# Kernel optimization log

Hardware: AMD Instinct MI355X
Metric: run time of the kernel (lower is better)

## Reference

```python
import jax, jax.numpy as jnp
import numpy as np

NUM_HEADS = 8
ATTENTION_SPAN = 128
LOOKAHEAD = True
NEG_INF = -1e9  # tf.keras Softmax mask adder


def setup_inputs() -> dict:
    key = jax.random.key(0)
    k1, k2, k3 = jax.random.split(key, 3)
    B, S, D = 4, 2048, 512
    x = jax.random.normal(k1, (B, S, D), dtype=jnp.float32)
    w_qkv = jax.random.normal(k2, (D, 3 * D), dtype=jnp.float32) * (D ** -0.5)
    w_proj = jax.random.normal(k3, (D, D), dtype=jnp.float32) * (D ** -0.5)
    return {"x": x, "w_qkv": w_qkv, "w_proj": w_proj}


def _band_mask(S: int) -> jnp.ndarray:
    idx = jnp.arange(S)
    m = jnp.abs(idx[None, :] - idx[:, None]) <= ATTENTION_SPAN
    if not LOOKAHEAD:
        m = m & (idx[None, :] <= idx[:, None])
    return m  # [S, S] bool


def reference(x, w_qkv, w_proj):
    B, S, D = x.shape
    H = NUM_HEADS
    hd = D // H
    scale = D ** -0.5  # NOTE: source scales by full dim, not head_dim

    qkv = x @ w_qkv                                   # [B,S,3D]
    qkv = qkv.reshape(B, S, H, 3 * hd).transpose(0, 2, 1, 3)  # [B,H,S,3hd]
    q, k, v = jnp.split(qkv, 3, axis=-1)              # each [B,H,S,hd]

    scores = jnp.einsum('bhqd,bhkd->bhqk', q, k) * scale  # [B,H,S,S]
    mask = _band_mask(S)[None, None, :, :]
    scores = scores + (1.0 - mask.astype(scores.dtype)) * NEG_INF
    attn = jax.nn.softmax(scores, axis=-1)

    out = jnp.einsum('bhqk,bhkd->bhqd', attn, v)      # [B,H,S,hd]
    out = out.transpose(0, 2, 1, 3).reshape(B, S, D)
    return out @ w_proj
```

## Files before the change

### kernel.cpp

```cpp
#include <hip/hip_runtime.h>

typedef unsigned short u16;
typedef unsigned long long u64;
typedef __attribute__((ext_vector_type(8))) short s16x8;
typedef __attribute__((ext_vector_type(4))) float f32x4;

#define MFMA16(a, b, c) __builtin_amdgcn_mfma_f32_16x16x32_bf16((a), (b), (c), 0, 0, 0)

__device__ __forceinline__ u16 f2bf(float f) {
  unsigned u = __float_as_uint(f);
  u += 0x7fffu + ((u >> 16) & 1u);
  return (u16)(u >> 16);
}

__device__ __forceinline__ void gld_lds16(const void* g, void* l) {
  __builtin_amdgcn_global_load_lds(
      (const __attribute__((address_space(1))) void*)g,
      (__attribute__((address_space(3))) void*)l, 16, 0, 0);
}

__global__ __launch_bounds__(256) void prep(const float* __restrict__ X,
                                            const float* __restrict__ Wqkv,
                                            const float* __restrict__ Wproj,
                                            u16* __restrict__ Xb,
                                            u16* __restrict__ wqT,
                                            u16* __restrict__ wpT) {
  const int bid = blockIdx.x;
  if (bid < 2048) {
    size_t idx = (size_t)bid * 256 + threadIdx.x;
    const float4 f0 = *(const float4*)(X + idx * 8);
    const float4 f1 = *(const float4*)(X + idx * 8 + 4);
    float fs[8] = {f0.x, f0.y, f0.z, f0.w, f1.x, f1.y, f1.z, f1.w};
    s16x8 hv;
#pragma unroll
    for (int j = 0; j < 8; ++j) hv[j] = (short)f2bf(fs[j]);
    *(s16x8*)(Xb + idx * 8) = hv;
  } else if (bid < 2432) {
    int idx = (bid - 2048) * 256 + threadIdx.x;
    int n = idx % 1536;
    int kc = idx / 1536;
    int t = n >> 9, ct = n & 511, h = ct >> 6, d = ct & 63;
    int src_c = h * 192 + t * 64 + d;
    s16x8 hv;
#pragma unroll
    for (int i = 0; i < 8; ++i) hv[i] = (short)f2bf(Wqkv[(size_t)(kc * 8 + i) * 1536 + src_c]);
    *(s16x8*)(wqT + (size_t)n * 512 + (size_t)kc * 8) = hv;
  } else {
    int idx = (bid - 2432) * 256 + threadIdx.x;
    int n = idx % 512;
    int kc = idx / 512;
    s16x8 hv;
#pragma unroll
    for (int i = 0; i < 8; ++i) hv[i] = (short)f2bf(Wproj[(size_t)(kc * 8 + i) * 512 + n]);
    *(s16x8*)(wpT + (size_t)n * 512 + (size_t)kc * 8) = hv;
  }
}

template <int EPI, int NCOL>
__global__ __launch_bounds__(256, 2) void gemm_bf16(
    const u16* __restrict__ A, const u16* __restrict__ B,
    float* __restrict__ OUT,
    u16* __restrict__ qo, u16* __restrict__ ko, u16* __restrict__ vto) {
  __shared__ u16 LDS[32768];
  u16* SA = LDS;
  u16* SB = LDS + 16384;
  const int tid = threadIdx.x;
  const int w = tid >> 6, lane = tid & 63;
  const int l15 = lane & 15, l4 = lane >> 4;
  const int bid0 = blockIdx.x;
  const int work = (bid0 & 7) * (8 * NCOL) + (bid0 >> 3);
  const int bx = work / NCOL;
  const int by = work % NCOL;
  const int row0 = bx * 128;
  const int col0 = by * 128;
  const int wr = w >> 1, wc = w & 1;

  const int lrow = lane >> 3, lslot = lane & 7;
  const int srcoff = lrow * 1024 + ((lslot ^ lrow) << 4);
  const char* pA = (const char*)A + (size_t)(row0 + w * 32) * 1024 + srcoff;
  const char* pB = (const char*)B + (size_t)(col0 + w * 32) * 1024 + srcoff;
  u16* sAw = SA + (w * 32) * 64;
  u16* sBw = SB + (w * 32) * 64;

#define STAGE(t_, b_)                                               \
  do {                                                              \
    const int kbb = (t_)*128;                                       \
    _Pragma("unroll")                                               \
    for (int j = 0; j < 4; ++j) {                                   \
      gld_lds16(pA + j * 8192 + kbb, sAw + (b_)*8192 + j * 512);    \
      gld_lds16(pB + j * 8192 + kbb, sBw + (b_)*8192 + j * 512);    \
    }                                                               \
  } while (0)

  const f32x4 fz = {0.f, 0.f, 0.f, 0.f};
  f32x4 acc[4][4];
  for (int a = 0; a < 4; ++a)
    for (int b = 0; b < 4; ++b) acc[a][b] = fz;

  STAGE(0, 0);
  asm volatile("s_waitcnt vmcnt(0)" ::: "memory");
  __builtin_amdgcn_sched_barrier(0);
  __builtin_amdgcn_s_barrier();

  for (int t = 0; t < 8; ++t) {
    const int cur = t & 1;
    if (t + 1 < 8) STAGE(t + 1, cur ^ 1);
#pragma unroll
    for (int ks = 0; ks < 2; ++ks) {
      s16x8 af[4], bf[4];
#pragma unroll
      for (int mi = 0; mi < 4; ++mi) {
        const int r = wr * 64 + mi * 16 + l15;
        const int sl = (ks * 4 + l4) ^ (r & 7);
        af[mi] = *(const s16x8*)&SA[cur * 8192 + r * 64 + sl * 8];
      }
#pragma unroll
      for (int nj = 0; nj < 4; ++nj) {
        const int r = wc * 64 + nj * 16 + l15;
        const int sl = (ks * 4 + l4) ^ (r & 7);
        bf[nj] = *(const s16x8*)&SB[cur * 8192 + r * 64 + sl * 8];
      }
      __builtin_amdgcn_s_setprio(1);
#pragma unroll
      for (int nj = 0; nj < 4; ++nj)
#pragma unroll
        for (int mi = 0; mi < 4; ++mi) acc[mi][nj] = MFMA16(af[mi], bf[nj], acc[mi][nj]);
      __builtin_amdgcn_s_setprio(0);
    }
    if (t < 7) {
      asm volatile("s_waitcnt vmcnt(0)" ::: "memory");
      __builtin_amdgcn_sched_barrier(0);
      __builtin_amdgcn_s_barrier();
    }
  }
#undef STAGE

  if (EPI == 0) {
#pragma unroll
    for (int mi = 0; mi < 4; ++mi)
#pragma unroll
      for (int nj = 0; nj < 4; ++nj)
#pragma unroll
        for (int rg = 0; rg < 4; ++rg) {
          int r_g = row0 + wr * 64 + mi * 16 + l4 * 4 + rg;
          int c_g = col0 + wc * 64 + nj * 16 + l15;
          OUT[(size_t)r_g * 512 + c_g] = acc[mi][nj][rg];
        }
    return;
  }

  const int b = row0 >> 11, srow = row0 & 2047;
  if (by < 8) {
    const int isq = (by < 4);
    const float QS = 0.06375874f;
    u16* dst = isq ? qo : ko;
#pragma unroll
    for (int mi = 0; mi < 4; ++mi)
#pragma unroll
      for (int nj = 0; nj < 4; ++nj)
#pragma unroll
        for (int rg = 0; rg < 4; ++rg) {
          float v = acc[mi][nj][rg];
          if (isq) v *= QS;
          int s = srow + wr * 64 + mi * 16 + l4 * 4 + rg;
          int ct = ((by & 3) * 128 + wc * 64 + nj * 16 + l15);
          int h = ct >> 6, d = ct & 63;
          dst[(((size_t)b * 8 + h) * 2048 + s) * 64 + d] = f2bf(v);
        }
  } else {
    const int vb = by - 8;
#pragma unroll
    for (int h = 0; h < 2; ++h) {
      __syncthreads();
      if (wc == h) {
#pragma unroll
        for (int mi = 0; mi < 4; ++mi)
#pragma unroll
          for (int nj = 0; nj < 4; ++nj)
#pragma unroll
            for (int rg = 0; rg < 4; ++rg) {
              int cl = nj * 16 + l15;
              int s = wr * 64 + mi * 16 + l4 * 4 + rg;
              LDS[cl * 130 + s] = f2bf(acc[mi][nj][rg]);
            }
      }
      __syncthreads();
      const unsigned* LDSw = (const unsigned*)LDS;
      int cl = tid >> 2, sh = tid & 3;
      int ct = vb * 128 + h * 64 + cl;
      int hd = ct >> 6, d = ct & 63;
      size_t o = (((size_t)b * 8 + hd) * 64 + d) * 2048 + srow + sh * 32;
      unsigned wbuf[16];
#pragma unroll
      for (int p = 0; p < 16; ++p) wbuf[p] = LDSw[cl * 65 + sh * 16 + p];
#pragma unroll
      for (int j = 0; j < 4; ++j) {
        uint4 u = {wbuf[j * 4], wbuf[j * 4 + 1], wbuf[j * 4 + 2], wbuf[j * 4 + 3]};
        *(uint4*)(vto + o + j * 8) = u;
      }
    }
  }
}

__global__ __launch_bounds__(512, 4) void attn_kernel(
    const u16* __restrict__ q, const u16* __restrict__ k,
    const u16* __restrict__ vt, u16* __restrict__ ao) {
  __shared__ u16 KT[3][64 * 64];
  __shared__ u16 VT[3][64 * 64];
  __shared__ u16 PT[8][16 * 64];
  const int tid = threadIdx.x;
  const int w = tid >> 6, lane = tid & 63;
  const int l15 = lane & 15, l4 = lane >> 4;
  const int bid0 = blockIdx.x;
  const int bid = (bid0 & 7) * 64 + (bid0 >> 3);
  const int qt = bid & 15, hh = (bid >> 4) & 7, b = bid >> 7;
  const size_t base = (size_t)(b * 8 + hh) * 2048 * 64;
  const int q0 = qt * 128 + w * 16;

  s16x8 qf[2];
#pragma unroll
  for (int ks = 0; ks < 2; ++ks)
    qf[ks] = *(const s16x8*)(q + base + (size_t)(q0 + l15) * 64 + ks * 32 + l4 * 8);

  const f32x4 fz = {0.f, 0.f, 0.f, 0.f};
  f32x4 O[4];
  for (int nd = 0; nd < 4; ++nd) O[nd] = fz;
  float l_sum = 0.f;

  const int lrow = lane >> 3, lslot = lane & 7;
  const int swzb = (lslot ^ lrow) << 4;
  const char* pK = (const char*)(k + base) + (w * 8 + lrow) * 128 + swzb;
  const char* pV = (const char*)(vt + base) + (size_t)(w * 8 + lrow) * 4096 + swzb;
  u16* dK = &KT[0][0] + w * 512;
  u16* dV = &VT[0][0] + w * 512;
  u16* phw = &PT[w][0];
  const int pswz = (l15 & 7) << 3;

#define STAGE(c_, b_)                                    \
  do {                                                   \
    gld_lds16(pK + (c_) * 8192, dK + (b_) * 4096);       \
    gld_lds16(pV + (c_) * 128,  dV + (b_) * 4096);       \
  } while (0)

  const int c0 = (2 * qt - 2) < 0 ? 0 : (2 * qt - 2);
  const int c1 = (2 * qt + 3) > 31 ? 31 : (2 * qt + 3);

  STAGE(c0, 0);
  STAGE(c0 + 1, 1);
  asm volatile("s_waitcnt vmcnt(2)" ::: "memory");
  __builtin_amdgcn_sched_barrier(0);
  __builtin_amdgcn_s_barrier();

  for (int c = c0; c <= c1; ++c) {
    const int buf = (c - c0) % 3;
    if (c + 2 <= c1) STAGE(c + 2, (c - c0 + 2) % 3);
    const int kb = c * 64;
    const bool skip = (kb - (q0 + 15) > 128) || (q0 - (kb + 63) > 128);
    if (!skip) {
      f32x4 S[4];
      for (int nj = 0; nj < 4; ++nj) S[nj] = fz;
      __builtin_amdgcn_s_setprio(1);
#pragma unroll
      for (int nj = 0; nj < 4; ++nj) {
        const int r = nj * 16 + l15;
#pragma unroll
        for (int ks = 0; ks < 2; ++ks) {
          const int sl = (ks * 4 + l4) ^ (r & 7);
          s16x8 kf = *(const s16x8*)&KT[buf][r * 64 + sl * 8];
          S[nj] = MFMA16(kf, qf[ks], S[nj]);
        }
      }
      __builtin_amdgcn_s_setprio(0);
      const bool needmask = (kb + 63 - q0 > 128) || (q0 + 15 - kb > 128);
      const int qrow = q0 + l15;
#pragma unroll
      for (int nj = 0; nj < 4; ++nj) {
        float p[4];
#pragma unroll
        for (int rg = 0; rg < 4; ++rg) {
          const int key = kb + nj * 16 + l4 * 4 + rg;
          float pp = exp2f(S[nj][rg]);
          if (needmask) {
            int dd = key - qrow;
            if (dd > 128 || dd < -128) pp = 0.f;
          }
          l_sum += pp;
          p[rg] = pp;
        }
        unsigned w0 = (unsigned)f2bf(p[0]) | ((unsigned)f2bf(p[1]) << 16);
        unsigned w1 = (unsigned)f2bf(p[2]) | ((unsigned)f2bf(p[3]) << 16);
        u64 pk = ((u64)w1 << 32) | (u64)w0;
        const int kbase = (nj * 16 + l4 * 4) ^ pswz;
        *(u64*)&phw[l15 * 64 + kbase] = pk;
      }
      __builtin_amdgcn_s_setprio(1);
#pragma unroll
      for (int ksp = 0; ksp < 2; ++ksp) {
        const int kbase = (ksp * 32 + l4 * 8) ^ pswz;
        s16x8 pa = *(const s16x8*)&phw[l15 * 64 + kbase];
#pragma unroll
        for (int nd = 0; nd < 4; ++nd) {
          const int r = nd * 16 + l15;
          const int sl = (ksp * 4 + l4) ^ (r & 7);
          s16x8 vf = *(const s16x8*)&VT[buf][r * 64 + sl * 8];
          O[nd] = MFMA16(pa, vf, O[nd]);
        }
      }
      __builtin_amdgcn_s_setprio(0);
    }
    if (c < c1) {
      if (c + 2 <= c1) {
        asm volatile("s_waitcnt vmcnt(2)" ::: "memory");
      } else {
        asm volatile("s_waitcnt vmcnt(0)" ::: "memory");
      }
      __builtin_amdgcn_sched_barrier(0);
      __builtin_amdgcn_s_barrier();
    }
  }
#undef STAGE

  l_sum += __shfl_xor(l_sum, 16);
  l_sum += __shfl_xor(l_sum, 32);
  float linv = 1.0f / l_sum;
#pragma unroll
  for (int rg = 0; rg < 4; ++rg) {
    const float inv = __shfl(linv, l4 * 4 + rg);
    const int s_g = q0 + l4 * 4 + rg;
#pragma unroll
    for (int nd = 0; nd < 4; ++nd) {
      float v = O[nd][rg] * inv;
      const int c_g = hh * 64 + nd * 16 + l15;
      ao[((size_t)b * 2048 + s_g) * 512 + c_g] = f2bf(v);
    }
  }
}

extern "C" void kernel_launch(void* const* d_in, const int* in_sizes, int n_in,
                              void* d_out, int out_size, void* d_ws, size_t ws_size,
                              hipStream_t stream) {
  const float* x = (const float*)d_in[0];
  const float* wqkv = (const float*)d_in[1];
  const float* wproj = (const float*)d_in[2];
  float* out = (float*)d_out;

  char* ws = (char*)d_ws;
  size_t off = 0;
  auto alloc = [&](size_t bytes) {
    void* p = ws + off;
    off += (bytes + 255) & ~(size_t)255;
    return p;
  };
  const size_t E = (size_t)4 * 8 * 2048 * 64;
  u16* Xb  = (u16*)alloc(E * 2);
  u16* qb  = (u16*)alloc(E * 2);
  u16* kb  = (u16*)alloc(E * 2);
  u16* vtb = (u16*)alloc(E * 2);
  u16* aob = (u16*)alloc(E * 2);
  u16* wqT = (u16*)alloc((size_t)1536 * 512 * 2);
  u16* wpT = (u16*)alloc((size_t)512 * 512 * 2);

  prep<<<dim3(2560), dim3(256), 0, stream>>>(x, wqkv, wproj, Xb, wqT, wpT);
  gemm_bf16<1, 12><<<dim3(768), dim3(256), 0, stream>>>(Xb, wqT, nullptr, qb, kb, vtb);
  attn_kernel<<<dim3(512), dim3(512), 0, stream>>>(qb, kb, vtb, aob);
  gemm_bf16<0, 4><<<dim3(256), dim3(256), 0, stream>>>(aob, wpT, out, nullptr, nullptr, nullptr);
}
```

Before: 58.81 us.

## Fuse fp32-to-bf16 conversion of X into the QKV GEMM A-tile loads

The separate prep pass that converts X to bf16 is removed. The QKV GEMM now loads fp32 X straight into registers, converts it to bf16 and writes the swizzled tile into LDS, while B still uses direct global-to-LDS loads. This avoids writing and re-reading a 16 MB bf16 copy of X and shrinks the prep launch. In exchange the GEMM reads twice as many A bytes, and each of the 12 column tiles converts the same rows again. The register-path conversion also adds VALU work and an extra lgkm wait before each barrier.

```diff
diff --git a/kernel.cpp b/kernel.cpp
--- a/kernel.cpp
+++ b/kernel.cpp
@@ -19,24 +19,13 @@
       (__attribute__((address_space(3))) void*)l, 16, 0, 0);
 }
 
-__global__ __launch_bounds__(256) void prep(const float* __restrict__ X,
-                                            const float* __restrict__ Wqkv,
+__global__ __launch_bounds__(256) void prep(const float* __restrict__ Wqkv,
                                             const float* __restrict__ Wproj,
-                                            u16* __restrict__ Xb,
                                             u16* __restrict__ wqT,
                                             u16* __restrict__ wpT) {
   const int bid = blockIdx.x;
-  if (bid < 2048) {
-    size_t idx = (size_t)bid * 256 + threadIdx.x;
-    const float4 f0 = *(const float4*)(X + idx * 8);
-    const float4 f1 = *(const float4*)(X + idx * 8 + 4);
-    float fs[8] = {f0.x, f0.y, f0.z, f0.w, f1.x, f1.y, f1.z, f1.w};
-    s16x8 hv;
-#pragma unroll
-    for (int j = 0; j < 8; ++j) hv[j] = (short)f2bf(fs[j]);
-    *(s16x8*)(Xb + idx * 8) = hv;
-  } else if (bid < 2432) {
-    int idx = (bid - 2048) * 256 + threadIdx.x;
+  if (bid < 384) {
+    int idx = bid * 256 + threadIdx.x;
     int n = idx % 1536;
     int kc = idx / 1536;
     int t = n >> 9, ct = n & 511, h = ct >> 6, d = ct & 63;
@@ -46,7 +35,7 @@
     for (int i = 0; i < 8; ++i) hv[i] = (short)f2bf(Wqkv[(size_t)(kc * 8 + i) * 1536 + src_c]);
     *(s16x8*)(wqT + (size_t)n * 512 + (size_t)kc * 8) = hv;
   } else {
-    int idx = (bid - 2432) * 256 + threadIdx.x;
+    int idx = (bid - 384) * 256 + threadIdx.x;
     int n = idx % 512;
     int kc = idx / 512;
     s16x8 hv;
@@ -58,6 +47,7 @@
 
 template <int EPI, int NCOL>
 __global__ __launch_bounds__(256, 2) void gemm_bf16(
+    const float* __restrict__ Xf,
     const u16* __restrict__ A, const u16* __restrict__ B,
     float* __restrict__ OUT,
     u16* __restrict__ qo, u16* __restrict__ ko, u16* __restrict__ vto) {
@@ -82,13 +72,45 @@
   u16* sAw = SA + (w * 32) * 64;
   u16* sBw = SB + (w * 32) * 64;
 
-#define STAGE(t_, b_)                                               \
+  const int arow = w * 32 + (lane >> 1);
+  const int ahalf = (lane & 1) * 32;
+  const float* pAf = Xf + (size_t)(row0 + arow) * 512 + ahalf;
+
+#define STAGE_B(t_, b_)                                             \
   do {                                                              \
     const int kbb = (t_)*128;                                       \
     _Pragma("unroll")                                               \
-    for (int j = 0; j < 4; ++j) {                                   \
+    for (int j = 0; j < 4; ++j)                                     \
+      gld_lds16(pB + j * 8192 + kbb, sBw + (b_)*8192 + j * 512);    \
+  } while (0)
+
+#define STAGE_A(t_, b_)                                             \
+  do {                                                              \
+    const int kbb = (t_)*128;                                       \
+    _Pragma("unroll")                                               \
+    for (int j = 0; j < 4; ++j)                                     \
       gld_lds16(pA + j * 8192 + kbb, sAw + (b_)*8192 + j * 512);    \
-      gld_lds16(pB + j * 8192 + kbb, sBw + (b_)*8192 + j * 512);    \
+  } while (0)
+
+  float4 a_in[8];
+#define LOAD_AF(t_)                                                 \
+  do {                                                              \
+    _Pragma("unroll")                                               \
+    for (int j = 0; j < 8; ++j)                                     \
+      a_in[j] = *(const float4*)(pAf + (t_)*64 + j * 4);            \
+  } while (0)
+
+#define CONV_AF(b_)                                                 \
+  do {                                                              \
+    _Pragma("unroll")                                               \
+    for (int j2 = 0; j2 < 4; ++j2) {                                \
+      uint4 pk;                                                     \
+      pk.x = (unsigned)f2bf(a_in[j2 * 2].x) | ((unsigned)f2bf(a_in[j2 * 2].y) << 16);   \
+      pk.y = (unsigned)f2bf(a_in[j2 * 2].z) | ((unsigned)f2bf(a_in[j2 * 2].w) << 16);   \
+      pk.z = (unsigned)f2bf(a_in[j2 * 2 + 1].x) | ((unsigned)f2bf(a_in[j2 * 2 + 1].y) << 16); \
+      pk.w = (unsigned)f2bf(a_in[j2 * 2 + 1].z) | ((unsigned)f2bf(a_in[j2 * 2 + 1].w) << 16); \
+      const int s = ((ahalf >> 3) + j2) ^ (arow & 7);               \
+      *(uint4*)&SA[(b_)*8192 + arow * 64 + s * 8] = pk;             \
     }                                                               \
   } while (0)
 
@@ -97,14 +119,35 @@
   for (int a = 0; a < 4; ++a)
     for (int b = 0; b < 4; ++b) acc[a][b] = fz;
 
-  STAGE(0, 0);
-  asm volatile("s_waitcnt vmcnt(0)" ::: "memory");
-  __builtin_amdgcn_sched_barrier(0);
-  __builtin_amdgcn_s_barrier();
+  if (EPI == 1) {
+    LOAD_AF(0);
+    STAGE_B(0, 0);
+    asm volatile("s_waitcnt vmcnt(0)" ::: "memory");
+    __builtin_amdgcn_sched_barrier(0);
+    CONV_AF(0);
+    asm volatile("s_waitcnt lgkmcnt(0)" ::: "memory");
+    __builtin_amdgcn_sched_barrier(0);
+    __builtin_amdgcn_s_barrier();
+  } else {
+    STAGE_A(0, 0);
+    STAGE_B(0, 0);
+    asm volatile("s_waitcnt vmcnt(0)" ::: "memory");
+    __builtin_amdgcn_sched_barrier(0);
+    __builtin_amdgcn_s_barrier();
+  }
 
   for (int t = 0; t < 8; ++t) {
     const int cur = t & 1;
-    if (t + 1 < 8) STAGE(t + 1, cur ^ 1);
+    if (t + 1 < 8) {
+      if (EPI == 1) {
+        LOAD_AF(t + 1);
+        STAGE_B(t + 1, cur ^ 1);
+      } else {
+        STAGE_A(t + 1, cur ^ 1);
+        STAGE_B(t + 1, cur ^ 1);
+      }
+      __builtin_amdgcn_sched_barrier(0);
+    }
 #pragma unroll
     for (int ks = 0; ks < 2; ++ks) {
       s16x8 af[4], bf[4];
@@ -130,10 +173,18 @@
     if (t < 7) {
       asm volatile("s_waitcnt vmcnt(0)" ::: "memory");
       __builtin_amdgcn_sched_barrier(0);
+      if (EPI == 1) {
+        CONV_AF(cur ^ 1);
+        asm volatile("s_waitcnt lgkmcnt(0)" ::: "memory");
+        __builtin_amdgcn_sched_barrier(0);
+      }
       __builtin_amdgcn_s_barrier();
     }
   }
-#undef STAGE
+#undef STAGE_A
+#undef STAGE_B
+#undef LOAD_AF
+#undef CONV_AF
 
   if (EPI == 0) {
 #pragma unroll
@@ -352,7 +403,6 @@
     return p;
   };
   const size_t E = (size_t)4 * 8 * 2048 * 64;
-  u16* Xb  = (u16*)alloc(E * 2);
   u16* qb  = (u16*)alloc(E * 2);
   u16* kb  = (u16*)alloc(E * 2);
   u16* vtb = (u16*)alloc(E * 2);
@@ -360,8 +410,8 @@
   u16* wqT = (u16*)alloc((size_t)1536 * 512 * 2);
   u16* wpT = (u16*)alloc((size_t)512 * 512 * 2);
 
-  prep<<<dim3(2560), dim3(256), 0, stream>>>(x, wqkv, wproj, Xb, wqT, wpT);
-  gemm_bf16<1, 12><<<dim3(768), dim3(256), 0, stream>>>(Xb, wqT, nullptr, qb, kb, vtb);
+  prep<<<dim3(512), dim3(256), 0, stream>>>(wqkv, wproj, wqT, wpT);
+  gemm_bf16<1, 12><<<dim3(768), dim3(256), 0, stream>>>(x, nullptr, wqT, nullptr, qb, kb, vtb);
   attn_kernel<<<dim3(512), dim3(512), 0, stream>>>(qb, kb, vtb, aob);
-  gemm_bf16<0, 4><<<dim3(256), dim3(256), 0, stream>>>(aob, wpT, out, nullptr, nullptr, nullptr);
-}
+  gemm_bf16<0, 4><<<dim3(256), dim3(256), 0, stream>>>(nullptr, aob, wpT, out, nullptr, nullptr, nullptr);
+}
```

New measurement: 79.68 us. +35.5%, slower.
